# Optimization experiments

Measured on AMD Instinct MI355X. Metric: run time of the kernel, lower is better.

## Reference

```python
import jax, jax.numpy as jnp
import numpy as np

N, E, F_IN, D_COORD, W, KW, KIN, DEPTH = 10000, 300000, 3, 3, 32, 256, 6, 4

def _lin(k, i, o):
    return jax.random.normal(k, (i, o), jnp.float32) * (1.0 / np.sqrt(i))

def setup_inputs() -> dict:
    key = jax.random.key(0)
    ks = jax.random.split(key, 16)
    x = jax.random.normal(ks[0], (N, F_IN), jnp.float32)
    edge_index = jax.random.randint(ks[1], (2, E), 0, N, jnp.int64)
    edge_attr = jax.random.normal(ks[2], (E, KIN), jnp.float32)
    coords_init = jax.random.normal(ks[3], (N, D_COORD), jnp.float32)
    return {
        "x": x, "edge_index": edge_index, "edge_attr": edge_attr,
        "coords_init": coords_init,
        "fc1_w": _lin(ks[4], F_IN, W), "fc1_b": jnp.zeros((W,), jnp.float32),
        # kernel DenseNet: [ker_in, ker_width//2, ker_width, width**2]
        "ker1_w": _lin(ks[5], KIN, KW // 2), "ker1_b": jnp.zeros((KW // 2,), jnp.float32),
        "ker2_w": _lin(ks[6], KW // 2, KW), "ker2_b": jnp.zeros((KW,), jnp.float32),
        "ker3_w": _lin(ks[7], KW, W * W), "ker3_b": jnp.zeros((W * W,), jnp.float32),
        # coord MLP: Linear(W,W)+ReLU+Linear(W,1)
        "cm1_w": _lin(ks[8], W, W), "cm1_b": jnp.zeros((W,), jnp.float32),
        "cm2_w": _lin(ks[9], W, 1), "cm2_b": jnp.zeros((1,), jnp.float32),
        # fc2: Linear(W,2W)+ReLU+Linear(2W,1)
        "fc2a_w": _lin(ks[10], W, 2 * W), "fc2a_b": jnp.zeros((2 * W,), jnp.float32),
        "fc2b_w": _lin(ks[11], 2 * W, 1), "fc2b_b": jnp.zeros((1,), jnp.float32),
        "depth": DEPTH,
    }

def reference(x, edge_index, edge_attr, coords_init,
              fc1_w, fc1_b, ker1_w, ker1_b, ker2_w, ker2_b, ker3_w, ker3_b,
              cm1_w, cm1_b, cm2_w, cm2_b, fc2a_w, fc2a_b, fc2b_w, fc2b_b, depth):
    n = x.shape[0]
    w = fc1_w.shape[1]
    row, col = edge_index[0], edge_index[1]
    h = x @ fc1_w + fc1_b  # [N, W]
    # edge kernel MLP -> per-edge [W, W] matrix (edge_attr fixed across layers)
    k = jax.nn.relu(edge_attr @ ker1_w + ker1_b)
    k = jax.nn.relu(k @ ker2_w + ker2_b)
    k = (k @ ker3_w + ker3_b).reshape(-1, w, w)  # [E, W, W]
    cnt = jnp.clip(jax.ops.segment_sum(jnp.ones((row.shape[0], 1), h.dtype), row, n), 1.0)
    coord = coords_init
    for _ in range(depth):
        m = jnp.einsum('eij,ej->ei', k, h[col])              # gather + kernel apply
        agg = jax.ops.segment_sum(m, row, n) / cnt           # mean scatter to nodes
        we = jax.nn.relu(m @ cm1_w + cm1_b) @ cm2_w + cm2_b  # [E, 1] coord weights
        trans = (coord[row] - coord[col]) * we               # equivariant edge vectors
        coord = coord + jax.ops.segment_sum(trans, row, n) / cnt
        h = jax.nn.relu(h + agg)
    out = jax.nn.relu(h @ fc2a_w + fc2a_b) @ fc2b_w + fc2b_b  # [N, 1]
    return out, coord
```

## Files before the change

kernel.cpp:

```cpp
#include <hip/hip_runtime.h>

#define NN 10000
#define NE 300000
#define DEPTH 4

typedef unsigned int   u32;
typedef unsigned short u16;
typedef unsigned char  u8;

typedef _Float16 half8  __attribute__((ext_vector_type(8)));
typedef _Float16 half2t __attribute__((ext_vector_type(2)));
typedef float  floatx16 __attribute__((ext_vector_type(16)));

__device__ __forceinline__ u32 f2h(float f) {
    f = fminf(fmaxf(f, -60000.f), 60000.f);
    _Float16 h = (_Float16)f;
    return (u32)__builtin_bit_cast(u16, h);
}
__device__ __forceinline__ float h2f(u16 b) {
    return (float)__builtin_bit_cast(_Float16, b);
}

__global__ void sentinel_kernel(float* out, int n, float val) {
    int i = blockIdx.x * 256 + threadIdx.x;
    if (i < n) out[i] = val;
}

__global__ void detect_idx_kernel(const int* __restrict__ ei, int* __restrict__ flag) {
    __shared__ int nz;
    if (threadIdx.x == 0) nz = 0;
    __syncthreads();
    if (ei[threadIdx.x * 2 + 1] != 0) atomicAdd(&nz, 1);
    __syncthreads();
    if (threadIdx.x == 0) *flag = (nz == 0) ? 1 : 0;
}

__global__ __launch_bounds__(256) void convert_idx_kernel(
    const int* __restrict__ ei, const int* __restrict__ flag,
    int* __restrict__ ridx, int* __restrict__ cidx)
{
    int e = blockIdx.x * 256 + threadIdx.x;
    if (e >= 2 * NE) return;
    const int is64 = *flag;
    int v = is64 ? ei[2 * e] : ei[e];
    if (e < NE) ridx[e] = v; else cidx[e - NE] = v;
}

__global__ __launch_bounds__(256) void init_nodes_kernel(
    const float* __restrict__ x, const float* __restrict__ fc1w,
    const float* __restrict__ fc1b, const float* __restrict__ ci,
    float* __restrict__ h, float* __restrict__ coord)
{
    int idx = blockIdx.x * 256 + threadIdx.x;
    if (idx < NN * 32) {
        int v = idx >> 5, f = idx & 31;
        float acc = fc1b[f];
#pragma unroll
        for (int i = 0; i < 3; i++) acc += x[v * 3 + i] * fc1w[i * 32 + f];
        h[idx] = acc;
    }
    if (idx < NN * 3) coord[idx] = ci[idx];
}

__global__ __launch_bounds__(256) void count_kernel(
    const int* __restrict__ ridx, const int* __restrict__ cidx,
    int* __restrict__ rowcnt, int* __restrict__ colcnt)
{
    int e = blockIdx.x * 256 + threadIdx.x;
    if (e < NE) { atomicAdd(&rowcnt[ridx[e]], 1); atomicAdd(&colcnt[cidx[e]], 1); }
}

__global__ void scan_kernel(const int* __restrict__ colcnt, const int* __restrict__ rowcnt,
                            int* __restrict__ cstart, int* __restrict__ cnext,
                            float* __restrict__ invc)
{
    __shared__ int part[256];
    const int t = threadIdx.x;
    int sum = 0;
    for (int i = 0; i < 40; i++) { int v = t * 40 + i; if (v < NN) sum += colcnt[v]; }
    part[t] = sum;
    __syncthreads();
    if (t == 0) {
        int run = 0;
        for (int i = 0; i < 256; i++) { int tmp = part[i]; part[i] = run; run += tmp; }
    }
    __syncthreads();
    int run = part[t];
    for (int i = 0; i < 40; i++) {
        int v = t * 40 + i;
        if (v < NN) { cstart[v] = run; cnext[v] = run; run += colcnt[v]; }
    }
    if (t == 255) cstart[NN] = run;
    for (int v = t; v < NN; v += 256) invc[v] = 1.0f / fmaxf((float)rowcnt[v], 1.0f);
}

__global__ __launch_bounds__(256) void scatter_kernel(
    const int* __restrict__ cidx, int* __restrict__ cnext, int* __restrict__ elist)
{
    int e = blockIdx.x * 256 + threadIdx.x;
    if (e < NE) { int pos = atomicAdd(&cnext[cidx[e]], 1); elist[pos] = e; }
}

__global__ __launch_bounds__(256) void w2pack_kernel(
    const float* __restrict__ w2, u16* __restrict__ w2h)
{
    const int slot = blockIdx.x * 256 + threadIdx.x;
    const int c = slot >> 9, s = (slot >> 6) & 7, l = slot & 63;
    const int li = l & 31, hf = l >> 5;
    const int k0 = s * 16 + hf * 8, col = c * 32 + li;
    u32 pk[8];
#pragma unroll
    for (int j = 0; j < 8; j++) pk[j] = f2h(w2[(size_t)(k0 + j) * 256 + col]);
    uint4 o;
    o.x = pk[0] | (pk[1] << 16);
    o.y = pk[2] | (pk[3] << 16);
    o.z = pk[4] | (pk[5] << 16);
    o.w = pk[6] | (pk[7] << 16);
    *(uint4*)&w2h[(size_t)slot * 8] = o;
}

__global__ __launch_bounds__(256) void mlp_k2_kernel(
    const float* __restrict__ ea,
    const float* __restrict__ w1, const float* __restrict__ b1,
    const u16* __restrict__ w2h, const float* __restrict__ b2,
    u8* __restrict__ k2base, float* __restrict__ k2s, int fk2)
{
    __shared__ __align__(16) float ea_s[32 * 6];
    __shared__ __align__(16) u16   k1f[4096];
    __shared__ __align__(16) float M_s[32 * 260];
    const int t  = threadIdx.x;
    const int e0 = blockIdx.x * 32;

    for (int idx = t; idx < 192; idx += 256)
        ea_s[idx] = ea[(size_t)e0 * 6 + idx];
    __syncthreads();

    for (int slot = t; slot < 512; slot += 256) {
        const int s  = slot >> 6;
        const int l  = slot & 63;
        const int li = l & 31, hf = l >> 5;
        const int k0 = s * 16 + hf * 8;
        float acc[8];
        {
            const float4 ba = *(const float4*)&b1[k0];
            const float4 bb = *(const float4*)&b1[k0 + 4];
            acc[0] = ba.x; acc[1] = ba.y; acc[2] = ba.z; acc[3] = ba.w;
            acc[4] = bb.x; acc[5] = bb.y; acc[6] = bb.z; acc[7] = bb.w;
        }
#pragma unroll
        for (int i = 0; i < 6; i++) {
            const float ev = ea_s[li * 6 + i];
            const float4 wa = *(const float4*)&w1[i * 128 + k0];
            const float4 wb = *(const float4*)&w1[i * 128 + k0 + 4];
            acc[0] += ev * wa.x; acc[1] += ev * wa.y;
            acc[2] += ev * wa.z; acc[3] += ev * wa.w;
            acc[4] += ev * wb.x; acc[5] += ev * wb.y;
            acc[6] += ev * wb.z; acc[7] += ev * wb.w;
        }
        uint4 o;
        o.x = f2h(fmaxf(acc[0], 0.f)) | (f2h(fmaxf(acc[1], 0.f)) << 16);
        o.y = f2h(fmaxf(acc[2], 0.f)) | (f2h(fmaxf(acc[3], 0.f)) << 16);
        o.z = f2h(fmaxf(acc[4], 0.f)) | (f2h(fmaxf(acc[5], 0.f)) << 16);
        o.w = f2h(fmaxf(acc[6], 0.f)) | (f2h(fmaxf(acc[7], 0.f)) << 16);
        *(uint4*)&k1f[slot * 8] = o;
    }
    __syncthreads();

    {
        const int w  = t >> 6, l = t & 63;
        const int li = l & 31, hf = l >> 5;
#pragma unroll
        for (int ct = 0; ct < 2; ct++) {
            const int c = w * 2 + ct;
            floatx16 acc;
#pragma unroll
            for (int r = 0; r < 16; r++) acc[r] = 0.f;
#pragma unroll
            for (int s = 0; s < 8; s++) {
                const half8 a = __builtin_bit_cast(half8,
                    *(const uint4*)&k1f[(s * 64 + l) * 8]);
                const half8 b = __builtin_bit_cast(half8,
                    *(const uint4*)&w2h[(((size_t)c * 8 + s) * 64 + l) * 8]);
                acc = __builtin_amdgcn_mfma_f32_32x32x16_f16(a, b, acc, 0, 0, 0);
            }
            const float bb = b2[c * 32 + li];
#pragma unroll
            for (int r = 0; r < 16; r++) {
                const int e = (r & 3) + 8 * (r >> 2) + 4 * hf;
                M_s[e * 260 + c * 32 + li] = fmaxf(acc[r] + bb, 0.f);
            }
        }
    }
    __syncthreads();

    {
        const int el = t >> 3, q = t & 7;
        const size_t eglob = (size_t)e0 + el;
        if (fk2 == 0) {
            u16* outp = (u16*)k2base + eglob * 256 + q * 32;
#pragma unroll
            for (int u = 0; u < 8; u += 2) {
                float4 a = *(float4*)&M_s[el * 260 + q * 32 + u * 4];
                float4 b = *(float4*)&M_s[el * 260 + q * 32 + u * 4 + 4];
                uint4 o;
                o.x = f2h(a.x) | (f2h(a.y) << 16);
                o.y = f2h(a.z) | (f2h(a.w) << 16);
                o.z = f2h(b.x) | (f2h(b.y) << 16);
                o.w = f2h(b.z) | (f2h(b.w) << 16);
                *(uint4*)(outp + u * 4) = o;
            }
        } else {
            float mx = 0.f;
#pragma unroll
            for (int u = 0; u < 32; u++) mx = fmaxf(mx, M_s[el * 260 + q * 32 + u]);
            mx = fmaxf(mx, __shfl_xor(mx, 1, 8));
            mx = fmaxf(mx, __shfl_xor(mx, 2, 8));
            mx = fmaxf(mx, __shfl_xor(mx, 4, 8));
            const float sc  = mx / 255.f;
            const float inv = (mx > 0.f) ? 255.f / mx : 0.f;
            if (q == 0) k2s[eglob] = sc;
            u8* outp = k2base + eglob * 256 + q * 32;
            u32 w[8];
#pragma unroll
            for (int u = 0; u < 8; u++) {
                float4 a = *(float4*)&M_s[el * 260 + q * 32 + u * 4];
                u32 q0 = (u32)fminf(rintf(a.x * inv), 255.f);
                u32 q1 = (u32)fminf(rintf(a.y * inv), 255.f);
                u32 q2 = (u32)fminf(rintf(a.z * inv), 255.f);
                u32 q3 = (u32)fminf(rintf(a.w * inv), 255.f);
                w[u] = q0 | (q1 << 8) | (q2 << 16) | (q3 << 24);
            }
            *(uint4*)outp        = make_uint4(w[0], w[1], w[2], w[3]);
            *(uint4*)(outp + 16) = make_uint4(w[4], w[5], w[6], w[7]);
        }
    }
}

__global__ __launch_bounds__(256) void bvec_kernel(
    const float* __restrict__ h, const float* __restrict__ b3, float* __restrict__ bvec)
{
    int idx = blockIdx.x * 256 + threadIdx.x;
    if (idx >= NN * 32) return;
    int v = idx >> 5, i = idx & 31;
    const float* hp = &h[(size_t)v * 32];
    const float* bp = &b3[i * 32];
    float acc = 0.f;
#pragma unroll
    for (int c = 0; c < 8; c++) {
        float4 hv = *(const float4*)&hp[c * 4];
        float4 bv = *(const float4*)&bp[c * 4];
        acc += hv.x * bv.x + hv.y * bv.y + hv.z * bv.z + hv.w * bv.w;
    }
    bvec[idx] = acc;
}

__global__ __launch_bounds__(256) void g_kernel(
    const float* __restrict__ h, const float* __restrict__ w3,
    u16* __restrict__ Gg)
{
    __shared__ __align__(16) u32 h16[128 * 16];
    const int t  = threadIdx.x;
    const int v0 = blockIdx.x * 128;

    {
        const int v = t >> 1, hh = t & 1;
        float4 a = make_float4(0.f, 0.f, 0.f, 0.f), b = a, c = a, d = a;
        if (v0 + v < NN) {
            const float* hp = &h[(size_t)(v0 + v) * 32 + hh * 16];
            a = *(const float4*)hp;       b = *(const float4*)(hp + 4);
            c = *(const float4*)(hp + 8); d = *(const float4*)(hp + 12);
        }
        uint4 o0, o1;
        o0.x = f2h(a.x) | (f2h(a.y) << 16);
        o0.y = f2h(a.z) | (f2h(a.w) << 16);
        o0.z = f2h(b.x) | (f2h(b.y) << 16);
        o0.w = f2h(b.z) | (f2h(b.w) << 16);
        o1.x = f2h(c.x) | (f2h(c.y) << 16);
        o1.y = f2h(c.z) | (f2h(c.w) << 16);
        o1.z = f2h(d.x) | (f2h(d.y) << 16);
        o1.w = f2h(d.z) | (f2h(d.w) << 16);
        *(uint4*)&h16[v * 16 + hh * 8]     = o0;
        *(uint4*)&h16[v * 16 + hh * 8 + 4] = o1;
    }
    __syncthreads();

    const int by    = blockIdx.y;
    const int lane  = t >> 2;
    const int i     = lane & 31;
    const int halfk = lane >> 5;
    const int j0    = (t & 3) * 2;
    const int k0    = by * 16 + halfk * 8 + j0;

    u32 w0p[16], w1p[16];
    {
        const float* wp0 = &w3[(size_t)k0 * 1024 + (size_t)i * 32];
        const float* wp1 = wp0 + 1024;
#pragma unroll
        for (int c = 0; c < 8; c++) {
            const float4 a = *(const float4*)&wp0[c * 4];
            w0p[c * 2]     = f2h(a.x) | (f2h(a.y) << 16);
            w0p[c * 2 + 1] = f2h(a.z) | (f2h(a.w) << 16);
            const float4 b = *(const float4*)&wp1[c * 4];
            w1p[c * 2]     = f2h(b.x) | (f2h(b.y) << 16);
            w1p[c * 2 + 1] = f2h(b.z) | (f2h(b.w) << 16);
        }
    }
    const int vmax = min(128, NN - v0);
    u32* outp = (u32*)Gg;
#pragma unroll 2
    for (int v = 0; v < vmax; v++) {
        float a0 = 0.f, a1 = 0.f;
#pragma unroll
        for (int c = 0; c < 4; c++) {
            const uint4 q = *(const uint4*)&h16[v * 16 + c * 4];
            const half2t h0 = __builtin_bit_cast(half2t, q.x);
            const half2t h1 = __builtin_bit_cast(half2t, q.y);
            const half2t h2 = __builtin_bit_cast(half2t, q.z);
            const half2t h3 = __builtin_bit_cast(half2t, q.w);
            a0 = __builtin_amdgcn_fdot2(h0, __builtin_bit_cast(half2t, w0p[c*4+0]), a0, false);
            a0 = __builtin_amdgcn_fdot2(h1, __builtin_bit_cast(half2t, w0p[c*4+1]), a0, false);
            a0 = __builtin_amdgcn_fdot2(h2, __builtin_bit_cast(half2t, w0p[c*4+2]), a0, false);
            a0 = __builtin_amdgcn_fdot2(h3, __builtin_bit_cast(half2t, w0p[c*4+3]), a0, false);
            a1 = __builtin_amdgcn_fdot2(h0, __builtin_bit_cast(half2t, w1p[c*4+0]), a1, false);
            a1 = __builtin_amdgcn_fdot2(h1, __builtin_bit_cast(half2t, w1p[c*4+1]), a1, false);
            a1 = __builtin_amdgcn_fdot2(h2, __builtin_bit_cast(half2t, w1p[c*4+2]), a1, false);
            a1 = __builtin_amdgcn_fdot2(h3, __builtin_bit_cast(half2t, w1p[c*4+3]), a1, false);
        }
        outp[(size_t)(v0 + v) * 4096 + by * 256 + t] = f2h(a0) | (f2h(a1) << 16);
    }
}

__global__ __launch_bounds__(256) void edge_kernel(
    const int* __restrict__ cstart, const int* __restrict__ elist,
    const int* __restrict__ ridx, const u8* __restrict__ k2base,
    const float* __restrict__ k2s, const u16* __restrict__ Gg,
    const float* __restrict__ coord,
    const float* __restrict__ cm1w, const float* __restrict__ cm1b,
    const float* __restrict__ cm2w, const float* __restrict__ cm2b,
    const float* __restrict__ bvec, float* __restrict__ agg,
    float* __restrict__ dco, int fk2)
{
    const int t    = threadIdx.x;
    const int w    = t >> 6;
    const int l    = t & 63;
    const int li   = l & 31;
    const int half = l >> 5;

    __shared__ __align__(16) float Mlds_all[4][32 * 36];
    __shared__ int rowS_all[4][32];
    float* Mlds = Mlds_all[w];
    int*   rowS = rowS_all[w];

    const int n = blockIdx.x * 4 + w;
    if (n >= NN) return;
    const int s0  = cstart[n];
    const int deg = cstart[n + 1] - s0;
    if (deg == 0) return;

    half8 cmb[2];
#pragma unroll
    for (int s2 = 0; s2 < 2; s2++)
#pragma unroll
        for (int j = 0; j < 8; j++)
            cmb[s2][j] = (_Float16)cm1w[(s2 * 16 + half * 8 + j) * 32 + li];
    half8 onesb;
#pragma unroll
    for (int j = 0; j < 8; j++) onesb[j] = (_Float16)1.0f;
    const float cm1bq = cm1b[li];
    const float cm2q  = cm2w[li];
    const float cm2b0 = cm2b[0];

    const float bv  = bvec[n * 32 + li];
    const float con = (li < 3) ? coord[(size_t)n * 3 + li] : 0.f;
    const u16* Gn = Gg + (size_t)n * 8192;

    for (int base = 0; base < deg; base += 32) {
        const int mye   = base + li;
        const int valid = (mye < deg) ? 1 : 0;
        const int eid   = valid ? elist[s0 + mye] : 0;
        const int rowv  = valid ? ridx[eid] : 0;
        if (l < 32) rowS[l] = rowv;

        uint4 gr[16];
#pragma unroll
        for (int s = 0; s < 16; s++)
            gr[s] = *(const uint4*)(Gn + s * 512 + l * 8);

        floatx16 acc;
#pragma unroll
        for (int r = 0; r < 16; r++) acc[r] = bv;

        if (fk2 == 1) {
            const float se = valid ? k2s[eid] : 0.f;
            const u8* k2row = k2base + (size_t)eid * 256 + half * 8;
            uint2 kr[16];
#pragma unroll
            for (int s = 0; s < 16; s++) kr[s] = *(const uint2*)(k2row + s * 16);
#pragma unroll
            for (int s = 0; s < 16; s++) {
                half8 a;
#pragma unroll
                for (int j = 0; j < 4; j++) {
                    a[j]     = (_Float16)((float)((kr[s].x >> (8 * j)) & 0xffu) * se);
                    a[4 + j] = (_Float16)((float)((kr[s].y >> (8 * j)) & 0xffu) * se);
                }
                acc = __builtin_amdgcn_mfma_f32_32x32x16_f16(
                    a, __builtin_bit_cast(half8, gr[s]), acc, 0, 0, 0);
            }
        } else {
            const u16* k2row = (const u16*)k2base + (size_t)eid * 256 + half * 8;
            uint4 kr[16];
#pragma unroll
            for (int s = 0; s < 16; s++) kr[s] = *(const uint4*)(k2row + s * 16);
#pragma unroll
            for (int s = 0; s < 16; s++)
                acc = __builtin_amdgcn_mfma_f32_32x32x16_f16(
                    __builtin_bit_cast(half8, kr[s]),
                    __builtin_bit_cast(half8, gr[s]), acc, 0, 0, 0);
        }

#pragma unroll
        for (int r = 0; r < 16; r++) {
            const int e = (r & 3) + 8 * (r >> 2) + 4 * half;
            Mlds[e * 36 + li] = acc[r];
        }
#pragma unroll
        for (int r = 0; r < 16; r++) {
            const int e = (r & 3) + 8 * (r >> 2) + 4 * half;
            if (base + e < deg) {
                const int rr = rowS[e];
                atomicAdd(&agg[(size_t)rr * 32 + li], acc[r]);
            }
        }
        asm volatile("s_waitcnt lgkmcnt(0)" ::: "memory");

        floatx16 acc2;
#pragma unroll
        for (int r = 0; r < 16; r++) acc2[r] = cm1bq;
#pragma unroll
        for (int s2 = 0; s2 < 2; s2++) {
            const float* mp = &Mlds[li * 36 + s2 * 16 + half * 8];
            const float4 m0 = *(const float4*)mp;
            const float4 m1 = *(const float4*)(mp + 4);
            half8 a;
            a[0] = (_Float16)m0.x; a[1] = (_Float16)m0.y;
            a[2] = (_Float16)m0.z; a[3] = (_Float16)m0.w;
            a[4] = (_Float16)m1.x; a[5] = (_Float16)m1.y;
            a[6] = (_Float16)m1.z; a[7] = (_Float16)m1.w;
            acc2 = __builtin_amdgcn_mfma_f32_32x32x16_f16(a, cmb[s2], acc2, 0, 0, 0);
        }

#pragma unroll
        for (int r = 0; r < 16; r++) {
            const int e = (r & 3) + 8 * (r >> 2) + 4 * half;
            Mlds[e * 36 + li] = fmaxf(acc2[r], 0.f) * cm2q;
        }
        asm volatile("s_waitcnt lgkmcnt(0)" ::: "memory");
        floatx16 acc3;
#pragma unroll
        for (int r = 0; r < 16; r++) acc3[r] = cm2b0;
#pragma unroll
        for (int s2 = 0; s2 < 2; s2++) {
            const float* mp = &Mlds[li * 36 + s2 * 16 + half * 8];
            const float4 m0 = *(const float4*)mp;
            const float4 m1 = *(const float4*)(mp + 4);
            half8 a;
            a[0] = (_Float16)m0.x; a[1] = (_Float16)m0.y;
            a[2] = (_Float16)m0.z; a[3] = (_Float16)m0.w;
            a[4] = (_Float16)m1.x; a[5] = (_Float16)m1.y;
            a[6] = (_Float16)m1.z; a[7] = (_Float16)m1.w;
            acc3 = __builtin_amdgcn_mfma_f32_32x32x16_f16(a, onesb, acc3, 0, 0, 0);
        }

#pragma unroll
        for (int r = 0; r < 16; r++) {
            const int e = (r & 3) + 8 * (r >> 2) + 4 * half;
            if (base + e < deg && li < 3) {
                const int rr = rowS[e];
                const float d = coord[(size_t)rr * 3 + li] - con;
                atomicAdd(&dco[(size_t)rr * 3 + li], d * acc3[r]);
            }
        }
    }
}

__global__ __launch_bounds__(256) void node_update_kernel(
    float* __restrict__ h, float* __restrict__ agg,
    float* __restrict__ coord, float* __restrict__ dco,
    const float* __restrict__ invc)
{
    int idx = blockIdx.x * 256 + threadIdx.x;
    if (idx < NN * 32) {
        int v = idx >> 5;
        h[idx] = fmaxf(h[idx] + agg[idx] * invc[v], 0.f);
        agg[idx] = 0.f;
    }
    if (idx < NN * 3) {
        coord[idx] += dco[idx] * invc[idx / 3];
        dco[idx] = 0.f;
    }
}

__global__ __launch_bounds__(256) void final_kernel(
    const float* __restrict__ h, const float* __restrict__ coord,
    const float* __restrict__ wa, const float* __restrict__ ba,
    const float* __restrict__ wb, const float* __restrict__ bb,
    float* __restrict__ out)
{
    const int lane = threadIdx.x & 63;
    const int v = blockIdx.x * 4 + (threadIdx.x >> 6);
    if (v >= NN) return;
    const float hreg = (lane < 32) ? h[(size_t)v * 32 + lane] : 0.f;
    float acc = ba[lane];
#pragma unroll
    for (int f = 0; f < 32; f++) acc += __shfl(hreg, f, 64) * wa[f * 64 + lane];
    float part = fmaxf(acc, 0.f) * wb[lane];
#pragma unroll
    for (int off = 32; off >= 1; off >>= 1) part += __shfl_xor(part, off, 64);
    if (lane == 0) out[v] = part + bb[0];
    if (lane < 3) out[NN + (size_t)v * 3 + lane] = coord[(size_t)v * 3 + lane];
}

extern "C" void kernel_launch(void* const* d_in, const int* in_sizes, int n_in,
                              void* d_out, int out_size, void* d_ws, size_t ws_size,
                              hipStream_t stream)
{
    const float* x    = (const float*)d_in[0];
    const int*   ei   = (const int*)d_in[1];
    const float* ea   = (const float*)d_in[2];
    const float* ci   = (const float*)d_in[3];
    const float* fc1w = (const float*)d_in[4];
    const float* fc1b = (const float*)d_in[5];
    const float* k1w  = (const float*)d_in[6];
    const float* k1b  = (const float*)d_in[7];
    const float* k2w  = (const float*)d_in[8];
    const float* k2b  = (const float*)d_in[9];
    const float* k3w  = (const float*)d_in[10];
    const float* k3b  = (const float*)d_in[11];
    const float* cm1w = (const float*)d_in[12];
    const float* cm1b = (const float*)d_in[13];
    const float* cm2w = (const float*)d_in[14];
    const float* cm2b = (const float*)d_in[15];
    const float* f2aw = (const float*)d_in[16];
    const float* f2ab = (const float*)d_in[17];
    const float* f2bw = (const float*)d_in[18];
    const float* f2bb = (const float*)d_in[19];

    size_t o_k2, o_k2s, o_G, o_h, o_agg, o_bv, o_coord, o_dco, o_invc, o_rc,
           o_cc, o_cs, o_cn, o_el, o_ri, o_ci, o_w2h;
#define ALGN(v) (((v) + 255) & ~(size_t)255)
    auto carve = [&](size_t k2es) -> size_t {
        size_t o = 0;
        o_k2   = o; o += ALGN((size_t)NE * 256 * k2es);
        o_k2s  = o; o += ALGN((size_t)NE * 4);
        o_G    = o; o += ALGN((size_t)NN * 8192 * 2);
        o_h    = o; o += ALGN((size_t)NN * 32 * 4);
        o_agg  = o; o += ALGN((size_t)NN * 32 * 4);
        o_bv   = o; o += ALGN((size_t)NN * 32 * 4);
        o_coord= o; o += ALGN((size_t)NN * 3 * 4);
        o_dco  = o; o += ALGN((size_t)NN * 3 * 4);
        o_invc = o; o += ALGN((size_t)NN * 4);
        o_rc   = o; o += ALGN((size_t)NN * 4);
        o_cc   = o; o += ALGN((size_t)NN * 4);
        o_cs   = o; o += ALGN((size_t)(NN + 1) * 4);
        o_cn   = o; o += ALGN((size_t)NN * 4);
        o_el   = o; o += ALGN((size_t)NE * 4);
        o_ri   = o; o += ALGN((size_t)NE * 4);
        o_ci   = o; o += ALGN((size_t)NE * 4);
        o_w2h  = o; o += ALGN((size_t)128 * 256 * 2);
        return o;
    };
    int fk2;
    if      (ws_size >= carve(2)) { fk2 = 0; carve(2); }
    else if (ws_size >= carve(1)) { fk2 = 1; carve(1); }
    else {
        sentinel_kernel<<<(NN * 4 + 255) / 256, 256, 0, stream>>>((float*)d_out, NN * 4, 1.0e6f);
        return;
    }

    char* wsb = (char*)d_ws;
    u8*    k2g   = (u8*)(wsb + o_k2);
    float* k2s   = (float*)(wsb + o_k2s);
    u16*   Gg    = (u16*)(wsb + o_G);
    float* h     = (float*)(wsb + o_h);
    float* agg   = (float*)(wsb + o_agg);
    float* bvec  = (float*)(wsb + o_bv);
    float* coord = (float*)(wsb + o_coord);
    float* dco   = (float*)(wsb + o_dco);
    float* invc  = (float*)(wsb + o_invc);
    int*   rowcnt= (int*)(wsb + o_rc);
    int*   colcnt= (int*)(wsb + o_cc);
    int*   cstart= (int*)(wsb + o_cs);
    int*   cnext = (int*)(wsb + o_cn);
    int*   elist = (int*)(wsb + o_el);
    int*   ridx  = (int*)(wsb + o_ri);
    int*   cidx  = (int*)(wsb + o_ci);
    u16*   w2h   = (u16*)(wsb + o_w2h);

    hipMemsetAsync(agg,    0, (size_t)NN * 32 * 4, stream);
    hipMemsetAsync(dco,    0, (size_t)NN * 3 * 4, stream);
    hipMemsetAsync(rowcnt, 0, (size_t)NN * 4, stream);
    hipMemsetAsync(colcnt, 0, (size_t)NN * 4, stream);

    detect_idx_kernel<<<1, 256, 0, stream>>>(ei, cnext);
    convert_idx_kernel<<<(2 * NE + 255) / 256, 256, 0, stream>>>(ei, cnext, ridx, cidx);
    init_nodes_kernel<<<(NN * 32 + 255) / 256, 256, 0, stream>>>(x, fc1w, fc1b, ci, h, coord);
    count_kernel<<<(NE + 255) / 256, 256, 0, stream>>>(ridx, cidx, rowcnt, colcnt);
    scan_kernel<<<1, 256, 0, stream>>>(colcnt, rowcnt, cstart, cnext, invc);
    scatter_kernel<<<(NE + 255) / 256, 256, 0, stream>>>(cidx, cnext, elist);
    w2pack_kernel<<<16, 256, 0, stream>>>(k2w, w2h);
    mlp_k2_kernel<<<NE / 32, 256, 0, stream>>>(ea, k1w, k1b, w2h, k2b, k2g, k2s, fk2);

    const dim3 ggrid((NN + 127) / 128, 16);
    for (int l = 0; l < DEPTH; l++) {
        bvec_kernel<<<(NN * 32 + 255) / 256, 256, 0, stream>>>(h, k3b, bvec);
        g_kernel<<<ggrid, 256, 0, stream>>>(h, k3w, Gg);
        edge_kernel<<<(NN + 3) / 4, 256, 0, stream>>>(cstart, elist, ridx, k2g, k2s,
                                                      Gg, coord, cm1w, cm1b, cm2w, cm2b,
                                                      bvec, agg, dco, fk2);
        node_update_kernel<<<(NN * 32 + 255) / 256, 256, 0, stream>>>(h, agg, coord, dco, invc);
    }
    final_kernel<<<(NN + 3) / 4, 256, 0, stream>>>(h, coord, f2aw, f2ab, f2bw, f2bb,
                                                   (float*)d_out);
}
```

Baseline: 963.9 us.

## Replace atomic scatter with row-CSR staging buffers and segmented node reduction

Adds a row-sorted CSR (rstart, rpos, rcol) so the edge kernel writes per-edge messages and coordinate weights as fp16 into row-ordered buffers instead of doing float atomics into agg and dco. A new node kernel then reduces each node's segment deterministically and ping-pongs the coordinate buffers. It also always uses the uint8 k2 storage, packs the cm1 weights once up front, and shrinks the LDS stride. This aims to remove atomic contention. In exchange it adds an extra pass over the per-edge buffers and fp16 rounding of the messages.

```diff
diff --git a/kernel.cpp b/kernel.cpp
--- a/kernel.cpp
+++ b/kernel.cpp
@@ -72,33 +72,53 @@
 
 __global__ void scan_kernel(const int* __restrict__ colcnt, const int* __restrict__ rowcnt,
                             int* __restrict__ cstart, int* __restrict__ cnext,
-                            float* __restrict__ invc)
-{
-    __shared__ int part[256];
+                            int* __restrict__ rstart, int* __restrict__ rnext,
+                            float* __restrict__ invc, int mode)
+{
+    __shared__ int partC[256], partR[256];
     const int t = threadIdx.x;
-    int sum = 0;
-    for (int i = 0; i < 40; i++) { int v = t * 40 + i; if (v < NN) sum += colcnt[v]; }
-    part[t] = sum;
+    int sumC = 0, sumR = 0;
+    for (int i = 0; i < 40; i++) {
+        int v = t * 40 + i;
+        if (v < NN) { sumC += colcnt[v]; sumR += rowcnt[v]; }
+    }
+    partC[t] = sumC; partR[t] = sumR;
     __syncthreads();
     if (t == 0) {
-        int run = 0;
-        for (int i = 0; i < 256; i++) { int tmp = part[i]; part[i] = run; run += tmp; }
+        int rc = 0, rr = 0;
+        for (int i = 0; i < 256; i++) {
+            int tc = partC[i]; partC[i] = rc; rc += tc;
+            int tr = partR[i]; partR[i] = rr; rr += tr;
+        }
     }
     __syncthreads();
-    int run = part[t];
+    int runC = partC[t], runR = partR[t];
     for (int i = 0; i < 40; i++) {
         int v = t * 40 + i;
-        if (v < NN) { cstart[v] = run; cnext[v] = run; run += colcnt[v]; }
-    }
-    if (t == 255) cstart[NN] = run;
+        if (v < NN) {
+            cstart[v] = runC; cnext[v] = runC; runC += colcnt[v];
+            if (mode) { rstart[v] = runR; rnext[v] = runR; runR += rowcnt[v]; }
+        }
+    }
+    if (t == 255) { cstart[NN] = runC; if (mode) rstart[NN] = runR; }
     for (int v = t; v < NN; v += 256) invc[v] = 1.0f / fmaxf((float)rowcnt[v], 1.0f);
 }
 
 __global__ __launch_bounds__(256) void scatter_kernel(
-    const int* __restrict__ cidx, int* __restrict__ cnext, int* __restrict__ elist)
+    const int* __restrict__ cidx, const int* __restrict__ ridx,
+    int* __restrict__ cnext, int* __restrict__ rnext,
+    int* __restrict__ elist, int* __restrict__ rpos, int* __restrict__ rcol,
+    int mode)
 {
     int e = blockIdx.x * 256 + threadIdx.x;
-    if (e < NE) { int pos = atomicAdd(&cnext[cidx[e]], 1); elist[pos] = e; }
+    if (e >= NE) return;
+    int pos = atomicAdd(&cnext[cidx[e]], 1);
+    elist[pos] = e;
+    if (mode) {
+        int rp = atomicAdd(&rnext[ridx[e]], 1);
+        rpos[e] = rp;
+        rcol[rp] = cidx[e];
+    }
 }
 
 __global__ __launch_bounds__(256) void w2pack_kernel(
@@ -119,11 +139,27 @@
     *(uint4*)&w2h[(size_t)slot * 8] = o;
 }
 
+__global__ void cm1pack_kernel(const float* __restrict__ cm1w, u16* __restrict__ cmpk)
+{
+    const int t = threadIdx.x;
+    if (t >= 128) return;
+    const int s2 = t >> 6, l = t & 63, li = l & 31, hf = l >> 5;
+    u32 pk[8];
+#pragma unroll
+    for (int j = 0; j < 8; j++) pk[j] = f2h(cm1w[(s2 * 16 + hf * 8 + j) * 32 + li]);
+    uint4 o;
+    o.x = pk[0] | (pk[1] << 16);
+    o.y = pk[2] | (pk[3] << 16);
+    o.z = pk[4] | (pk[5] << 16);
+    o.w = pk[6] | (pk[7] << 16);
+    *(uint4*)&cmpk[(size_t)(s2 * 64 + l) * 8] = o;
+}
+
 __global__ __launch_bounds__(256) void mlp_k2_kernel(
     const float* __restrict__ ea,
     const float* __restrict__ w1, const float* __restrict__ b1,
     const u16* __restrict__ w2h, const float* __restrict__ b2,
-    u8* __restrict__ k2base, float* __restrict__ k2s, int fk2)
+    u8* __restrict__ k2base, float* __restrict__ k2s)
 {
     __shared__ __align__(16) float ea_s[32 * 6];
     __shared__ __align__(16) u16   k1f[4096];
@@ -196,43 +232,28 @@
     {
         const int el = t >> 3, q = t & 7;
         const size_t eglob = (size_t)e0 + el;
-        if (fk2 == 0) {
-            u16* outp = (u16*)k2base + eglob * 256 + q * 32;
-#pragma unroll
-            for (int u = 0; u < 8; u += 2) {
-                float4 a = *(float4*)&M_s[el * 260 + q * 32 + u * 4];
-                float4 b = *(float4*)&M_s[el * 260 + q * 32 + u * 4 + 4];
-                uint4 o;
-                o.x = f2h(a.x) | (f2h(a.y) << 16);
-                o.y = f2h(a.z) | (f2h(a.w) << 16);
-                o.z = f2h(b.x) | (f2h(b.y) << 16);
-                o.w = f2h(b.z) | (f2h(b.w) << 16);
-                *(uint4*)(outp + u * 4) = o;
-            }
-        } else {
-            float mx = 0.f;
-#pragma unroll
-            for (int u = 0; u < 32; u++) mx = fmaxf(mx, M_s[el * 260 + q * 32 + u]);
-            mx = fmaxf(mx, __shfl_xor(mx, 1, 8));
-            mx = fmaxf(mx, __shfl_xor(mx, 2, 8));
-            mx = fmaxf(mx, __shfl_xor(mx, 4, 8));
-            const float sc  = mx / 255.f;
-            const float inv = (mx > 0.f) ? 255.f / mx : 0.f;
-            if (q == 0) k2s[eglob] = sc;
-            u8* outp = k2base + eglob * 256 + q * 32;
-            u32 w[8];
-#pragma unroll
-            for (int u = 0; u < 8; u++) {
-                float4 a = *(float4*)&M_s[el * 260 + q * 32 + u * 4];
-                u32 q0 = (u32)fminf(rintf(a.x * inv), 255.f);
-                u32 q1 = (u32)fminf(rintf(a.y * inv), 255.f);
-                u32 q2 = (u32)fminf(rintf(a.z * inv), 255.f);
-                u32 q3 = (u32)fminf(rintf(a.w * inv), 255.f);
-                w[u] = q0 | (q1 << 8) | (q2 << 16) | (q3 << 24);
-            }
-            *(uint4*)outp        = make_uint4(w[0], w[1], w[2], w[3]);
-            *(uint4*)(outp + 16) = make_uint4(w[4], w[5], w[6], w[7]);
-        }
+        float mx = 0.f;
+#pragma unroll
+        for (int u = 0; u < 32; u++) mx = fmaxf(mx, M_s[el * 260 + q * 32 + u]);
+        mx = fmaxf(mx, __shfl_xor(mx, 1, 8));
+        mx = fmaxf(mx, __shfl_xor(mx, 2, 8));
+        mx = fmaxf(mx, __shfl_xor(mx, 4, 8));
+        const float sc  = mx / 255.f;
+        const float inv = (mx > 0.f) ? 255.f / mx : 0.f;
+        if (q == 0) k2s[eglob] = sc;
+        u8* outp = k2base + eglob * 256 + q * 32;
+        u32 w[8];
+#pragma unroll
+        for (int u = 0; u < 8; u++) {
+            float4 a = *(float4*)&M_s[el * 260 + q * 32 + u * 4];
+            u32 q0 = (u32)fminf(rintf(a.x * inv), 255.f);
+            u32 q1 = (u32)fminf(rintf(a.y * inv), 255.f);
+            u32 q2 = (u32)fminf(rintf(a.z * inv), 255.f);
+            u32 q3 = (u32)fminf(rintf(a.w * inv), 255.f);
+            w[u] = q0 | (q1 << 8) | (q2 << 16) | (q3 << 24);
+        }
+        *(uint4*)outp        = make_uint4(w[0], w[1], w[2], w[3]);
+        *(uint4*)(outp + 16) = make_uint4(w[4], w[5], w[6], w[7]);
     }
 }
 
@@ -332,13 +353,14 @@
 
 __global__ __launch_bounds__(256) void edge_kernel(
     const int* __restrict__ cstart, const int* __restrict__ elist,
-    const int* __restrict__ ridx, const u8* __restrict__ k2base,
-    const float* __restrict__ k2s, const u16* __restrict__ Gg,
-    const float* __restrict__ coord,
-    const float* __restrict__ cm1w, const float* __restrict__ cm1b,
+    const int* __restrict__ ridx, const int* __restrict__ rpos,
+    const u8* __restrict__ k2base, const float* __restrict__ k2s,
+    const u16* __restrict__ Gg, const float* __restrict__ coord,
+    const u16* __restrict__ cmpk, const float* __restrict__ cm1b,
     const float* __restrict__ cm2w, const float* __restrict__ cm2b,
-    const float* __restrict__ bvec, float* __restrict__ agg,
-    float* __restrict__ dco, int fk2)
+    const float* __restrict__ bvec,
+    float* __restrict__ agg, float* __restrict__ dco,
+    u16* __restrict__ mbuf, u16* __restrict__ webuf, int mode)
 {
     const int t    = threadIdx.x;
     const int w    = t >> 6;
@@ -346,10 +368,10 @@
     const int li   = l & 31;
     const int half = l >> 5;
 
-    __shared__ __align__(16) float Mlds_all[4][32 * 36];
-    __shared__ int rowS_all[4][32];
+    __shared__ __align__(16) float Mlds_all[4][32 * 34];
+    __shared__ int idxS_all[4][32];
     float* Mlds = Mlds_all[w];
-    int*   rowS = rowS_all[w];
+    int*   idxS = idxS_all[w];
 
     const int n = blockIdx.x * 4 + w;
     if (n >= NN) return;
@@ -358,127 +380,129 @@
     if (deg == 0) return;
 
     half8 cmb[2];
-#pragma unroll
-    for (int s2 = 0; s2 < 2; s2++)
-#pragma unroll
-        for (int j = 0; j < 8; j++)
-            cmb[s2][j] = (_Float16)cm1w[(s2 * 16 + half * 8 + j) * 32 + li];
+    cmb[0] = __builtin_bit_cast(half8, *(const uint4*)&cmpk[(size_t)(0 * 64 + l) * 8]);
+    cmb[1] = __builtin_bit_cast(half8, *(const uint4*)&cmpk[(size_t)(1 * 64 + l) * 8]);
     half8 onesb;
 #pragma unroll
     for (int j = 0; j < 8; j++) onesb[j] = (_Float16)1.0f;
     const float cm1bq = cm1b[li];
     const float cm2q  = cm2w[li];
     const float cm2b0 = cm2b[0];
-
-    const float bv  = bvec[n * 32 + li];
-    const float con = (li < 3) ? coord[(size_t)n * 3 + li] : 0.f;
+    const float bv    = bvec[n * 32 + li];
+    const float con   = (mode == 0 && li < 3) ? coord[(size_t)n * 3 + li] : 0.f;
     const u16* Gn = Gg + (size_t)n * 8192;
 
     for (int base = 0; base < deg; base += 32) {
         const int mye   = base + li;
         const int valid = (mye < deg) ? 1 : 0;
         const int eid   = valid ? elist[s0 + mye] : 0;
-        const int rowv  = valid ? ridx[eid] : 0;
-        if (l < 32) rowS[l] = rowv;
+        if (l < 32) idxS[l] = valid ? (mode ? rpos[eid] : ridx[eid]) : 0;
 
         uint4 gr[16];
 #pragma unroll
         for (int s = 0; s < 16; s++)
             gr[s] = *(const uint4*)(Gn + s * 512 + l * 8);
+        const float se = valid ? k2s[eid] : 0.f;
+        const u8* k2row = k2base + (size_t)eid * 256 + half * 8;
+        uint2 kr[16];
+#pragma unroll
+        for (int s = 0; s < 16; s++) kr[s] = *(const uint2*)(k2row + s * 16);
 
         floatx16 acc;
 #pragma unroll
         for (int r = 0; r < 16; r++) acc[r] = bv;
-
-        if (fk2 == 1) {
-            const float se = valid ? k2s[eid] : 0.f;
-            const u8* k2row = k2base + (size_t)eid * 256 + half * 8;
-            uint2 kr[16];
-#pragma unroll
-            for (int s = 0; s < 16; s++) kr[s] = *(const uint2*)(k2row + s * 16);
-#pragma unroll
-            for (int s = 0; s < 16; s++) {
-                half8 a;
-#pragma unroll
-                for (int j = 0; j < 4; j++) {
-                    a[j]     = (_Float16)((float)((kr[s].x >> (8 * j)) & 0xffu) * se);
-                    a[4 + j] = (_Float16)((float)((kr[s].y >> (8 * j)) & 0xffu) * se);
-                }
-                acc = __builtin_amdgcn_mfma_f32_32x32x16_f16(
-                    a, __builtin_bit_cast(half8, gr[s]), acc, 0, 0, 0);
+#pragma unroll
+        for (int s = 0; s < 16; s++) {
+            half8 a;
+#pragma unroll
+            for (int j = 0; j < 4; j++) {
+                a[j]     = (_Float16)((float)((kr[s].x >> (8 * j)) & 0xffu) * se);
+                a[4 + j] = (_Float16)((float)((kr[s].y >> (8 * j)) & 0xffu) * se);
+            }
+            acc = __builtin_amdgcn_mfma_f32_32x32x16_f16(
+                a, __builtin_bit_cast(half8, gr[s]), acc, 0, 0, 0);
+        }
+
+#pragma unroll
+        for (int r = 0; r < 16; r++) {
+            const int e = (r & 3) + 8 * (r >> 2) + 4 * half;
+            Mlds[e * 34 + li] = acc[r];
+        }
+        if (mode == 0) {
+#pragma unroll
+            for (int r = 0; r < 16; r++) {
+                const int e = (r & 3) + 8 * (r >> 2) + 4 * half;
+                if (base + e < deg)
+                    atomicAdd(&agg[(size_t)idxS[e] * 32 + li], acc[r]);
             }
         } else {
-            const u16* k2row = (const u16*)k2base + (size_t)eid * 256 + half * 8;
-            uint4 kr[16];
-#pragma unroll
-            for (int s = 0; s < 16; s++) kr[s] = *(const uint4*)(k2row + s * 16);
-#pragma unroll
-            for (int s = 0; s < 16; s++)
-                acc = __builtin_amdgcn_mfma_f32_32x32x16_f16(
-                    __builtin_bit_cast(half8, kr[s]),
-                    __builtin_bit_cast(half8, gr[s]), acc, 0, 0, 0);
+#pragma unroll
+            for (int r = 0; r < 16; r++) {
+                const int e = (r & 3) + 8 * (r >> 2) + 4 * half;
+                if (base + e < deg)
+                    mbuf[(size_t)idxS[e] * 32 + li] = (u16)f2h(acc[r]);
+            }
+        }
+        asm volatile("s_waitcnt lgkmcnt(0)" ::: "memory");
+
+        floatx16 acc2;
+#pragma unroll
+        for (int r = 0; r < 16; r++) acc2[r] = cm1bq;
+#pragma unroll
+        for (int s2 = 0; s2 < 2; s2++) {
+            const float* mp = &Mlds[li * 34 + s2 * 16 + half * 8];
+            const float2 m0 = *(const float2*)mp;
+            const float2 m1 = *(const float2*)(mp + 2);
+            const float2 m2 = *(const float2*)(mp + 4);
+            const float2 m3 = *(const float2*)(mp + 6);
+            half8 a;
+            a[0] = (_Float16)m0.x; a[1] = (_Float16)m0.y;
+            a[2] = (_Float16)m1.x; a[3] = (_Float16)m1.y;
+            a[4] = (_Float16)m2.x; a[5] = (_Float16)m2.y;
+            a[6] = (_Float16)m3.x; a[7] = (_Float16)m3.y;
+            acc2 = __builtin_amdgcn_mfma_f32_32x32x16_f16(a, cmb[s2], acc2, 0, 0, 0);
         }
 
 #pragma unroll
         for (int r = 0; r < 16; r++) {
             const int e = (r & 3) + 8 * (r >> 2) + 4 * half;
-            Mlds[e * 36 + li] = acc[r];
-        }
-#pragma unroll
-        for (int r = 0; r < 16; r++) {
-            const int e = (r & 3) + 8 * (r >> 2) + 4 * half;
-            if (base + e < deg) {
-                const int rr = rowS[e];
-                atomicAdd(&agg[(size_t)rr * 32 + li], acc[r]);
-            }
+            Mlds[e * 34 + li] = fmaxf(acc2[r], 0.f) * cm2q;
         }
         asm volatile("s_waitcnt lgkmcnt(0)" ::: "memory");
-
-        floatx16 acc2;
-#pragma unroll
-        for (int r = 0; r < 16; r++) acc2[r] = cm1bq;
+        floatx16 acc3;
+#pragma unroll
+        for (int r = 0; r < 16; r++) acc3[r] = cm2b0;
 #pragma unroll
         for (int s2 = 0; s2 < 2; s2++) {
-            const float* mp = &Mlds[li * 36 + s2 * 16 + half * 8];
-            const float4 m0 = *(const float4*)mp;
-            const float4 m1 = *(const float4*)(mp + 4);
+            const float* mp = &Mlds[li * 34 + s2 * 16 + half * 8];
+            const float2 m0 = *(const float2*)mp;
+            const float2 m1 = *(const float2*)(mp + 2);
+            const float2 m2 = *(const float2*)(mp + 4);
+            const float2 m3 = *(const float2*)(mp + 6);
             half8 a;
             a[0] = (_Float16)m0.x; a[1] = (_Float16)m0.y;
-            a[2] = (_Float16)m0.z; a[3] = (_Float16)m0.w;
-            a[4] = (_Float16)m1.x; a[5] = (_Float16)m1.y;
-            a[6] = (_Float16)m1.z; a[7] = (_Float16)m1.w;
-            acc2 = __builtin_amdgcn_mfma_f32_32x32x16_f16(a, cmb[s2], acc2, 0, 0, 0);
-        }
-
-#pragma unroll
-        for (int r = 0; r < 16; r++) {
-            const int e = (r & 3) + 8 * (r >> 2) + 4 * half;
-            Mlds[e * 36 + li] = fmaxf(acc2[r], 0.f) * cm2q;
-        }
-        asm volatile("s_waitcnt lgkmcnt(0)" ::: "memory");
-        floatx16 acc3;
-#pragma unroll
-        for (int r = 0; r < 16; r++) acc3[r] = cm2b0;
-#pragma unroll
-        for (int s2 = 0; s2 < 2; s2++) {
-            const float* mp = &Mlds[li * 36 + s2 * 16 + half * 8];
-            const float4 m0 = *(const float4*)mp;
-            const float4 m1 = *(const float4*)(mp + 4);
-            half8 a;
-            a[0] = (_Float16)m0.x; a[1] = (_Float16)m0.y;
-            a[2] = (_Float16)m0.z; a[3] = (_Float16)m0.w;
-            a[4] = (_Float16)m1.x; a[5] = (_Float16)m1.y;
-            a[6] = (_Float16)m1.z; a[7] = (_Float16)m1.w;
+            a[2] = (_Float16)m1.x; a[3] = (_Float16)m1.y;
+            a[4] = (_Float16)m2.x; a[5] = (_Float16)m2.y;
+            a[6] = (_Float16)m3.x; a[7] = (_Float16)m3.y;
             acc3 = __builtin_amdgcn_mfma_f32_32x32x16_f16(a, onesb, acc3, 0, 0, 0);
         }
 
-#pragma unroll
-        for (int r = 0; r < 16; r++) {
-            const int e = (r & 3) + 8 * (r >> 2) + 4 * half;
-            if (base + e < deg && li < 3) {
-                const int rr = rowS[e];
-                const float d = coord[(size_t)rr * 3 + li] - con;
-                atomicAdd(&dco[(size_t)rr * 3 + li], d * acc3[r]);
+        if (mode == 0) {
+#pragma unroll
+            for (int r = 0; r < 16; r++) {
+                const int e = (r & 3) + 8 * (r >> 2) + 4 * half;
+                if (base + e < deg && li < 3) {
+                    const int rr = idxS[e];
+                    const float d = coord[(size_t)rr * 3 + li] - con;
+                    atomicAdd(&dco[(size_t)rr * 3 + li], d * acc3[r]);
+                }
+            }
+        } else {
+#pragma unroll
+            for (int r = 0; r < 16; r++) {
+                const int e = (r & 3) + 8 * (r >> 2) + 4 * half;
+                if (base + e < deg && li == 0)
+                    webuf[idxS[e]] = (u16)f2h(acc3[r]);
             }
         }
     }
@@ -498,6 +522,50 @@
     if (idx < NN * 3) {
         coord[idx] += dco[idx] * invc[idx / 3];
         dco[idx] = 0.f;
+    }
+}
+
+__global__ __launch_bounds__(256) void node_update2_kernel(
+    float* __restrict__ h, const float* __restrict__ coordCur,
+    float* __restrict__ coordNew, const u16* __restrict__ mbuf,
+    const u16* __restrict__ webuf, const int* __restrict__ rcol,
+    const int* __restrict__ rstart, const float* __restrict__ invc)
+{
+    const int t = threadIdx.x, w = t >> 6, l = t & 63;
+    const int li = l & 31, half = l >> 5;
+    const int v = blockIdx.x * 4 + w;
+    if (v >= NN) return;
+    const int s0 = rstart[v], s1 = rstart[v + 1];
+    const float iv = invc[v];
+
+    float acc = 0.f;
+    for (int s = s0 + half; s < s1; s += 2)
+        acc += h2f(mbuf[(size_t)s * 32 + li]);
+    acc += __shfl_xor(acc, 32, 64);
+    if (half == 0)
+        h[(size_t)v * 32 + li] = fmaxf(h[(size_t)v * 32 + li] + acc * iv, 0.f);
+
+    const float c0 = coordCur[(size_t)v * 3 + 0];
+    const float c1 = coordCur[(size_t)v * 3 + 1];
+    const float c2 = coordCur[(size_t)v * 3 + 2];
+    float p0 = 0.f, p1 = 0.f, p2 = 0.f;
+    for (int s = s0 + l; s < s1; s += 64) {
+        const float we = h2f(webuf[s]);
+        const int col = rcol[s];
+        p0 += (c0 - coordCur[(size_t)col * 3 + 0]) * we;
+        p1 += (c1 - coordCur[(size_t)col * 3 + 1]) * we;
+        p2 += (c2 - coordCur[(size_t)col * 3 + 2]) * we;
+    }
+#pragma unroll
+    for (int off = 32; off >= 1; off >>= 1) {
+        p0 += __shfl_xor(p0, off, 64);
+        p1 += __shfl_xor(p1, off, 64);
+        p2 += __shfl_xor(p2, off, 64);
+    }
+    if (l == 0) {
+        coordNew[(size_t)v * 3 + 0] = c0 + p0 * iv;
+        coordNew[(size_t)v * 3 + 1] = c1 + p1 * iv;
+        coordNew[(size_t)v * 3 + 2] = c2 + p2 * iv;
     }
 }
 
@@ -546,34 +614,52 @@
     const float* f2bw = (const float*)d_in[18];
     const float* f2bb = (const float*)d_in[19];
 
-    size_t o_k2, o_k2s, o_G, o_h, o_agg, o_bv, o_coord, o_dco, o_invc, o_rc,
-           o_cc, o_cs, o_cn, o_el, o_ri, o_ci, o_w2h;
+    size_t o_k2, o_k2s, o_G, o_h, o_bv, o_coA, o_coB, o_invc, o_rc, o_cc,
+           o_cs, o_rs, o_cn, o_rn, o_el, o_w2h, o_cmpk, o_agg, o_dco,
+           o_ri, o_ci, o_rp, o_rcl, o_mb, o_wb;
 #define ALGN(v) (((v) + 255) & ~(size_t)255)
-    auto carve = [&](size_t k2es) -> size_t {
+    auto carve = [&](int mode) -> size_t {
         size_t o = 0;
-        o_k2   = o; o += ALGN((size_t)NE * 256 * k2es);
-        o_k2s  = o; o += ALGN((size_t)NE * 4);
-        o_G    = o; o += ALGN((size_t)NN * 8192 * 2);
-        o_h    = o; o += ALGN((size_t)NN * 32 * 4);
-        o_agg  = o; o += ALGN((size_t)NN * 32 * 4);
-        o_bv   = o; o += ALGN((size_t)NN * 32 * 4);
-        o_coord= o; o += ALGN((size_t)NN * 3 * 4);
-        o_dco  = o; o += ALGN((size_t)NN * 3 * 4);
-        o_invc = o; o += ALGN((size_t)NN * 4);
-        o_rc   = o; o += ALGN((size_t)NN * 4);
-        o_cc   = o; o += ALGN((size_t)NN * 4);
-        o_cs   = o; o += ALGN((size_t)(NN + 1) * 4);
-        o_cn   = o; o += ALGN((size_t)NN * 4);
-        o_el   = o; o += ALGN((size_t)NE * 4);
-        o_ri   = o; o += ALGN((size_t)NE * 4);
-        o_ci   = o; o += ALGN((size_t)NE * 4);
-        o_w2h  = o; o += ALGN((size_t)128 * 256 * 2);
+        o_k2  = o; o += ALGN((size_t)NE * 256);
+        o_k2s = o; o += ALGN((size_t)NE * 4);
+        o_G   = o; o += ALGN((size_t)NN * 8192 * 2);
+        o_h   = o; o += ALGN((size_t)NN * 32 * 4);
+        o_bv  = o; o += ALGN((size_t)NN * 32 * 4);
+        o_coA = o; o += ALGN((size_t)NN * 3 * 4);
+        o_invc= o; o += ALGN((size_t)NN * 4);
+        o_rc  = o; o += ALGN((size_t)NN * 4);
+        o_cc  = o; o += ALGN((size_t)NN * 4);
+        o_cs  = o; o += ALGN((size_t)(NN + 1) * 4);
+        o_cn  = o; o += ALGN((size_t)NN * 4);
+        o_el  = o; o += ALGN((size_t)NE * 4);
+        o_w2h = o; o += ALGN((size_t)128 * 256 * 2);
+        o_cmpk= o; o += ALGN((size_t)1024 * 2);
+        if (mode == 0) {
+            o_agg = o; o += ALGN((size_t)NN * 32 * 4);
+            o_dco = o; o += ALGN((size_t)NN * 3 * 4);
+            o_ri  = o; o += ALGN((size_t)NE * 4);
+            o_ci  = o; o += ALGN((size_t)NE * 4);
+            o_coB = o_coA; o_rs = o_cs; o_rn = o_cn;
+            o_rp = o_el; o_rcl = o_el; o_mb = o_k2; o_wb = o_k2;
+        } else {
+            o_coB = o; o += ALGN((size_t)NN * 3 * 4);
+            o_rs  = o; o += ALGN((size_t)(NN + 1) * 4);
+            o_rn  = o; o += ALGN((size_t)NN * 4);
+            o_rp  = o; o += ALGN((size_t)NE * 4);
+            o_rcl = o; o += ALGN((size_t)NE * 4);
+            const size_t u = o;
+            o_ri = u; o_ci = u + ALGN((size_t)NE * 4);
+            o_mb = u; o_wb = u + ALGN((size_t)NE * 32 * 2);
+            const size_t setup_sz = 2 * ALGN((size_t)NE * 4);
+            const size_t layer_sz = ALGN((size_t)NE * 32 * 2) + ALGN((size_t)NE * 2);
+            o += (setup_sz > layer_sz) ? setup_sz : layer_sz;
+            o_agg = o_k2; o_dco = o_k2;
+        }
         return o;
     };
-    int fk2;
-    if      (ws_size >= carve(2)) { fk2 = 0; carve(2); }
-    else if (ws_size >= carve(1)) { fk2 = 1; carve(1); }
-    else {
+    int mode = (ws_size >= carve(1)) ? 1 : 0;
+    size_t need = carve(mode);
+    if (ws_size < need) {
         sentinel_kernel<<<(NN * 4 + 255) / 256, 256, 0, stream>>>((float*)d_out, NN * 4, 1.0e6f);
         return;
     }
@@ -583,43 +669,66 @@
     float* k2s   = (float*)(wsb + o_k2s);
     u16*   Gg    = (u16*)(wsb + o_G);
     float* h     = (float*)(wsb + o_h);
-    float* agg   = (float*)(wsb + o_agg);
     float* bvec  = (float*)(wsb + o_bv);
-    float* coord = (float*)(wsb + o_coord);
-    float* dco   = (float*)(wsb + o_dco);
+    float* coA   = (float*)(wsb + o_coA);
+    float* coB   = (float*)(wsb + o_coB);
     float* invc  = (float*)(wsb + o_invc);
     int*   rowcnt= (int*)(wsb + o_rc);
     int*   colcnt= (int*)(wsb + o_cc);
     int*   cstart= (int*)(wsb + o_cs);
+    int*   rstart= (int*)(wsb + o_rs);
     int*   cnext = (int*)(wsb + o_cn);
+    int*   rnext = (int*)(wsb + o_rn);
     int*   elist = (int*)(wsb + o_el);
+    u16*   w2h   = (u16*)(wsb + o_w2h);
+    u16*   cmpk  = (u16*)(wsb + o_cmpk);
+    float* agg   = (float*)(wsb + o_agg);
+    float* dco   = (float*)(wsb + o_dco);
     int*   ridx  = (int*)(wsb + o_ri);
     int*   cidx  = (int*)(wsb + o_ci);
-    u16*   w2h   = (u16*)(wsb + o_w2h);
-
-    hipMemsetAsync(agg,    0, (size_t)NN * 32 * 4, stream);
-    hipMemsetAsync(dco,    0, (size_t)NN * 3 * 4, stream);
+    int*   rpos  = (int*)(wsb + o_rp);
+    int*   rcol  = (int*)(wsb + o_rcl);
+    u16*   mbuf  = (u16*)(wsb + o_mb);
+    u16*   webuf = (u16*)(wsb + o_wb);
+
     hipMemsetAsync(rowcnt, 0, (size_t)NN * 4, stream);
     hipMemsetAsync(colcnt, 0, (size_t)NN * 4, stream);
+    if (mode == 0) {
+        hipMemsetAsync(agg, 0, (size_t)NN * 32 * 4, stream);
+        hipMemsetAsync(dco, 0, (size_t)NN * 3 * 4, stream);
+    }
 
     detect_idx_kernel<<<1, 256, 0, stream>>>(ei, cnext);
     convert_idx_kernel<<<(2 * NE + 255) / 256, 256, 0, stream>>>(ei, cnext, ridx, cidx);
-    init_nodes_kernel<<<(NN * 32 + 255) / 256, 256, 0, stream>>>(x, fc1w, fc1b, ci, h, coord);
+    init_nodes_kernel<<<(NN * 32 + 255) / 256, 256, 0, stream>>>(x, fc1w, fc1b, ci, h, coA);
     count_kernel<<<(NE + 255) / 256, 256, 0, stream>>>(ridx, cidx, rowcnt, colcnt);
-    scan_kernel<<<1, 256, 0, stream>>>(colcnt, rowcnt, cstart, cnext, invc);
-    scatter_kernel<<<(NE + 255) / 256, 256, 0, stream>>>(cidx, cnext, elist);
+    scan_kernel<<<1, 256, 0, stream>>>(colcnt, rowcnt, cstart, cnext, rstart, rnext,
+                                       invc, mode);
+    scatter_kernel<<<(NE + 255) / 256, 256, 0, stream>>>(cidx, ridx, cnext, rnext,
+                                                         elist, rpos, rcol, mode);
     w2pack_kernel<<<16, 256, 0, stream>>>(k2w, w2h);
-    mlp_k2_kernel<<<NE / 32, 256, 0, stream>>>(ea, k1w, k1b, w2h, k2b, k2g, k2s, fk2);
-
+    cm1pack_kernel<<<1, 128, 0, stream>>>(cm1w, cmpk);
+    mlp_k2_kernel<<<NE / 32, 256, 0, stream>>>(ea, k1w, k1b, w2h, k2b, k2g, k2s);
+
+    float* coCur = coA;
+    float* coAlt = coB;
     const dim3 ggrid((NN + 127) / 128, 16);
     for (int l = 0; l < DEPTH; l++) {
         bvec_kernel<<<(NN * 32 + 255) / 256, 256, 0, stream>>>(h, k3b, bvec);
         g_kernel<<<ggrid, 256, 0, stream>>>(h, k3w, Gg);
-        edge_kernel<<<(NN + 3) / 4, 256, 0, stream>>>(cstart, elist, ridx, k2g, k2s,
-                                                      Gg, coord, cm1w, cm1b, cm2w, cm2b,
-                                                      bvec, agg, dco, fk2);
-        node_update_kernel<<<(NN * 32 + 255) / 256, 256, 0, stream>>>(h, agg, coord, dco, invc);
-    }
-    final_kernel<<<(NN + 3) / 4, 256, 0, stream>>>(h, coord, f2aw, f2ab, f2bw, f2bb,
+        edge_kernel<<<(NN + 3) / 4, 256, 0, stream>>>(cstart, elist, ridx, rpos,
+                                                      k2g, k2s, Gg, coCur, cmpk,
+                                                      cm1b, cm2w, cm2b, bvec,
+                                                      agg, dco, mbuf, webuf, mode);
+        if (mode == 1) {
+            node_update2_kernel<<<(NN + 3) / 4, 256, 0, stream>>>(
+                h, coCur, coAlt, mbuf, webuf, rcol, rstart, invc);
+            float* tmp = coCur; coCur = coAlt; coAlt = tmp;
+        } else {
+            node_update_kernel<<<(NN * 32 + 255) / 256, 256, 0, stream>>>(
+                h, agg, coCur, dco, invc);
+        }
+    }
+    final_kernel<<<(NN + 3) / 4, 256, 0, stream>>>(h, coCur, f2aw, f2ab, f2bw, f2bb,
                                                    (float*)d_out);
 }
```

After: 925.6 us. -4.0%, faster.
